# Kernel optimization log

Hardware: AMD Instinct MI355X
Metric: run time of the kernel (lower is better)

The kernel has to match this reference:

```python
import jax, jax.numpy as jnp
import numpy as np

W_CHAMFER = (1.0, 1.0, 1.0)
W_LAPLACE = 0.5
W_MOVE = 0.1
W_EDGE = 0.1
W_NORMAL = 1.6e-4
W_CONST = 1.0
LAP_CONST = (0.2, 1.0, 1.0)
EPS = 1e-12


def _normalize(x):
    # F.normalize(x, dim=-1): x / max(||x||, eps)
    n = jnp.sqrt(jnp.sum(x * x, axis=-1, keepdims=True))
    return x / jnp.maximum(n, EPS)


def _pairwise_sq(x, y):
    # x: (B,N,3), y: (B,M,3) -> (B,N,M) squared distances, GEMM form
    x2 = jnp.sum(x * x, -1)
    y2 = jnp.sum(y * y, -1)
    xy = jnp.einsum('bnd,bmd->bnm', x, y)
    return x2[:, :, None] + y2[:, None, :] - 2.0 * xy


def _laplace_coord(pts, lap_idx):
    # pts: (B,V,3); lap_idx: (V,10) = [8 neighbor idx (-1 invalid), self, count]
    idx = lap_idx[:, :8]
    mask = idx < 0
    safe = jnp.where(mask, 0, idx)
    nbrs = pts[:, safe]                                  # (B,V,8,3)
    nbrs = jnp.where(mask[None, :, :, None], 0.0, nbrs)
    count = lap_idx[:, -1].astype(pts.dtype)
    return pts - nbrs.sum(2) / count[None, :, None]


def setup_inputs():
    key = jax.random.key(0)
    B, M = 2, 8192
    Vs = (642, 2562, 10242)
    Es = (1920, 7680, 30720)
    ks = jax.random.split(key, 3 + 4 * 3)
    inp = {}
    inp['gt_coord'] = jax.random.normal(ks[0], (B, M, 3), jnp.float32)
    inp['gt_normal'] = _normalize(jax.random.normal(ks[1], (B, M, 3), jnp.float32))
    for i, (V, E) in enumerate(zip(Vs, Es)):
        k0, k1, k2, k3 = ks[3 + 4 * i], ks[4 + 4 * i], ks[5 + 4 * i], ks[6 + 4 * i]
        inp[f'pred_coord_{i}'] = jax.random.normal(k0, (B, V, 3), jnp.float32)
        inp[f'pred_before_{i}'] = inp[f'pred_coord_{i}'] + 0.05 * jax.random.normal(k1, (B, V, 3), jnp.float32)
        inp[f'edges_{i}'] = jax.random.randint(k2, (E, 2), 0, V)
        nbr = jax.random.randint(k3, (V, 8), 0, V)
        nbr = nbr.at[:, 6:].set(-1)                      # 6 valid neighbors, 2 invalid slots
        self_idx = jnp.arange(V)[:, None]
        count = jnp.full((V, 1), 6)
        inp[f'laplace_idx_{i}'] = jnp.concatenate([nbr, self_idx, count], axis=1)
    return inp


def reference(pred_coord_0, pred_coord_1, pred_coord_2, pred_before_0, pred_before_1, pred_before_2, gt_coord, gt_normal, laplace_idx_0, laplace_idx_1, laplace_idx_2, edges_0, edges_1, edges_2):
    preds = (pred_coord_0, pred_coord_1, pred_coord_2)
    befores = (pred_before_0, pred_before_1, pred_before_2)
    laps = (laplace_idx_0, laplace_idx_1, laplace_idx_2)
    edges_all = (edges_0, edges_1, edges_2)
    chamfer_loss = 0.0
    edge_loss = 0.0
    normal_loss = 0.0
    lap_loss = 0.0
    move_loss = 0.0
    for i in range(3):
        pred, before, lap_idx, edges = preds[i], befores[i], laps[i], edges_all[i]
        # shared pairwise distance matrix for chamfer + knn (original recomputes)
        d = _pairwise_sq(pred, gt_coord)                 # (B,V,M)
        chamfer_loss = chamfer_loss + W_CHAMFER[i] * (jnp.mean(jnp.min(d, axis=1)) + jnp.mean(jnp.min(d, axis=2)))
        knn_idx = jnp.argmin(d, axis=2)                  # (B,V): nearest gt per pred pt
        e0, e1 = edges[:, 0], edges[:, 1]
        evec = _normalize(pred[:, e0] - pred[:, e1])     # (B,E,3)
        # faithful to torch: knn.idx.flatten() then index_select -> only batch-0
        # indices ever selected since edge ids < V
        sel = knn_idx.reshape(-1)[e0]
        nrm = _normalize(gt_normal[:, sel])              # (B,E,3)
        normal_loss = normal_loss + jnp.mean(jnp.abs(jnp.sum(evec * nrm, axis=2)))
        edge_loss = edge_loss + 3.0 * jnp.mean((pred[:, e0] - pred[:, e1]) ** 2)
        l1 = _laplace_coord(before, lap_idx)
        l2 = _laplace_coord(pred, lap_idx)
        lap_loss = lap_loss + LAP_CONST[i] * 3.0 * jnp.mean((l1 - l2) ** 2)
        if i > 0:
            move_loss = move_loss + LAP_CONST[i] * 3.0 * jnp.mean((before - pred) ** 2)
    loss = chamfer_loss + W_LAPLACE * lap_loss + W_MOVE * move_loss + W_EDGE * edge_loss + W_NORMAL * normal_loss
    return W_CONST * loss
```

## Files before the change

kernel.cpp:

```cpp
#include <hip/hip_runtime.h>


#define DEV __device__ __forceinline__

typedef __attribute__((ext_vector_type(8))) short bs8;
typedef __attribute__((ext_vector_type(4))) float f32x4;

#define WS_GT   65536
#define WS_VP   1114112
#define WS_PA   2916352
#define WS_PB   6520832
#define WS_PAu  2916352
#define WS_PBu  3028992

DEV unsigned long long umin64(unsigned long long a, unsigned long long b) { return a < b ? a : b; }

DEV float blockReduceSum256(float v) {
    #pragma unroll
    for (int o = 32; o > 0; o >>= 1) v += __shfl_down(v, o, 64);
    __shared__ float red4[4];
    int wid = threadIdx.x >> 6;
    if ((threadIdx.x & 63) == 0) red4[wid] = v;
    __syncthreads();
    return (threadIdx.x == 0) ? (red4[0] + red4[1] + red4[2] + red4[3]) : 0.0f;
}

DEV void split3(float u, unsigned short& h, unsigned short& m, unsigned short& l) {
    unsigned a = __float_as_uint(u);
    h = (unsigned short)(a >> 16);
    float r1 = u - __uint_as_float(a & 0xFFFF0000u);
    unsigned bb = __float_as_uint(r1);
    m = (unsigned short)(bb >> 16);
    float r2 = r1 - __uint_as_float(bb & 0xFFFF0000u);
    l = (unsigned short)(__float_as_uint(r2) >> 16);
}

DEV void packGT(const float* __restrict__ gp, char* dst) {
    float x = gp[0], y = gp[1], z = gp[2];
    unsigned short hx,mx,lx, hy,my,ly, hz,mz,lz, nh,nm,nl;
    split3(x,hx,mx,lx); split3(y,hy,my,ly); split3(z,hz,mz,lz);
    float n = fmaf(x,x,fmaf(y,y,z*z));
    split3(n,nh,nm,nl);
    const short ONE = (short)0x3F80;
    bs8 w0 = {(short)hx,(short)hx,(short)mx,(short)hx,(short)lx,(short)mx,(short)hy,(short)hy};
    bs8 w1 = {(short)my,(short)hy,(short)ly,(short)my,(short)hz,(short)hz,(short)mz,(short)hz};
    bs8 w2 = {(short)lz,(short)mz,(short)nh,(short)nm,(short)nl,ONE,ONE,ONE};
    bs8 w3 = {0,0,0,0,0,0,0,0};
    *(bs8*)(dst)       = w0;
    *(bs8*)(dst + 256) = w1;
    *(bs8*)(dst + 512) = w2;
    *(bs8*)(dst + 768) = w3;
}

DEV void packVERT(const float* __restrict__ pp, char* dst) {
    float x = pp[0], y = pp[1], z = pp[2];
    unsigned short hx,mx,lx, hy,my,ly, hz,mz,lz, nh,nm,nl;
    split3(-2.f*x,hx,mx,lx); split3(-2.f*y,hy,my,ly); split3(-2.f*z,hz,mz,lz);
    float n = fmaf(x,x,fmaf(y,y,z*z));
    split3(n,nh,nm,nl);
    const short ONE = (short)0x3F80;
    bs8 w0 = {(short)hx,(short)mx,(short)hx,(short)lx,(short)hx,(short)mx,(short)hy,(short)my};
    bs8 w1 = {(short)hy,(short)ly,(short)hy,(short)my,(short)hz,(short)mz,(short)hz,(short)lz};
    bs8 w2 = {(short)hz,(short)mz,ONE,ONE,ONE,(short)nh,(short)nm,(short)nl};
    bs8 w3 = {0,0,0,0,0,0,0,0};
    *(bs8*)(dst)       = w0;
    *(bs8*)(dst + 256) = w1;
    *(bs8*)(dst + 512) = w2;
    *(bs8*)(dst + 768) = w3;
}

__global__ __launch_bounds__(256) void kPack(
    const float* __restrict__ p0, const float* __restrict__ p1, const float* __restrict__ p2,
    const float* __restrict__ gt, char* ws)
{
    int idx = blockIdx.x * 256 + threadIdx.x;
    if (idx < 16384) {
        packGT(gt + (size_t)idx * 3, ws + WS_GT + (size_t)(idx >> 4) * 1024 + (idx & 15) * 16);
    } else if (idx < 44544) {
        int s = idx - 16384;
        int b = s >= 14080 ? 1 : 0;
        int q = s - b * 14080;
        int V, padOff; const float* predL;
        if (q < 768)       { V = 642;   padOff = 0;    predL = p0; }
        else if (q < 3584) { V = 2562;  padOff = 768;  predL = p1; }
        else               { V = 10242; padOff = 3584; predL = p2; }
        int u = q - padOff;
        int v = u - (u >= V ? V : 0);
        packVERT(predL + ((size_t)b * V + v) * 3,
                 ws + WS_VP + (size_t)(s >> 4) * 1024 + (s & 15) * 16);
    }
}

template<bool B0>
DEV void mfmaLoop(const char* SA, const char* SB, char* VML,
                  float (&gmin)[4][4], int embedBase, unsigned embedMask)
{
    const int tid = threadIdx.x;
    const int w = tid >> 6, L = tid & 63, lr = L & 15, lg = L >> 4;
    const char* abase = SA + (w * 4) * 1024 + lg * 256 + lr * 16;
    bs8 af[4];
    #pragma unroll
    for (int g = 0; g < 4; g++) af[g] = *(const bs8*)(abase + g * 1024);
    const f32x4 zero = {0.f, 0.f, 0.f, 0.f};
    const char* bbase = SB + lg * 256 + lr * 16;
    bs8 bf = *(const bs8*)(bbase);
    #pragma unroll 2
    for (int vg = 0; vg < 16; vg++) {
        bs8 bfn = bf;
        if (vg < 15) bfn = *(const bs8*)(bbase + (vg + 1) * 1024);
        float vmin = 3.0e38f;
        int code = embedBase;
        #pragma unroll
        for (int gg = 0; gg < 4; gg++) {
            f32x4 acc = __builtin_amdgcn_mfma_f32_16x16x32_bf16(af[gg], bf, zero, 0, 0, 0);
            gmin[gg][0] = fminf(gmin[gg][0], acc[0]);
            gmin[gg][1] = fminf(gmin[gg][1], acc[1]);
            gmin[gg][2] = fminf(gmin[gg][2], acc[2]);
            gmin[gg][3] = fminf(gmin[gg][3], acc[3]);
            float t = fminf(fminf(acc[0], acc[1]), fminf(acc[2], acc[3]));
            if (B0) {
                t = fmaxf(t, 0.0f);
                t = __uint_as_float((__float_as_uint(t) & embedMask) | (unsigned)code);
                code += 4;
            }
            vmin = fminf(vmin, t);
        }
        vmin = fminf(vmin, __shfl_xor(vmin, 16));
        vmin = fminf(vmin, __shfl_xor(vmin, 32));
        if (lg == 0) *(float*)(VML + ((vg * 16 + lr) * 4 + w) * 4) = vmin;
        bf = bfn;
    }
}

template<bool STORE>
__global__ __launch_bounds__(256, 4) void kMega2(
    const float* __restrict__ p0, const float* __restrict__ p1, const float* __restrict__ p2,
    const float* __restrict__ b0p, const float* __restrict__ b1p, const float* __restrict__ b2p,
    const int* __restrict__ l0, const int* __restrict__ l1, const int* __restrict__ l2,
    char* ws)
{
    extern __shared__ char smem[];
    int bid = blockIdx.x;
    if (bid == 0 && threadIdx.x == 0) { *(float*)ws = 0.f; *(unsigned*)(ws + 4) = 0u; }
    if (bid < 128) {
        float c = 0.0f;
        int idx = bid * 256 + threadIdx.x;
        if (idx < 26892) {
            int level, V, t;
            const float *pred, *bef; const int* lap;
            if (idx < 1284)      { level = 0; V = 642;   pred = p0; bef = b0p; lap = l0; t = idx; }
            else if (idx < 6408) { level = 1; V = 2562;  pred = p1; bef = b1p; lap = l1; t = idx - 1284; }
            else                 { level = 2; V = 10242; pred = p2; bef = b2p; lap = l2; t = idx - 6408; }
            int b = t / V;
            int v = t - b * V;
            const float* P  = pred + ((size_t)b * V + v) * 3;
            const float* Bf = bef  + ((size_t)b * V + v) * 3;
            float dx = Bf[0] - P[0], dy = Bf[1] - P[1], dz = Bf[2] - P[2];
            float sx = 0.f, sy = 0.f, sz = 0.f;
            const int* Lp = lap + v * 10;
            #pragma unroll
            for (int j = 0; j < 8; j++) {
                int n = Lp[j];
                if (n >= 0) {
                    const float* Pn = pred + ((size_t)b * V + n) * 3;
                    const float* Bn = bef  + ((size_t)b * V + n) * 3;
                    sx += Bn[0] - Pn[0]; sy += Bn[1] - Pn[1]; sz += Bn[2] - Pn[2];
                }
            }
            float invc = 1.0f / (float)Lp[9];
            float lx = dx - sx * invc, ly = dy - sy * invc, lz = dz - sz * invc;
            float sl = fmaf(lx, lx, fmaf(ly, ly, lz * lz));
            float sm = fmaf(dx, dx, fmaf(dy, dy, dz * dz));
            float lapc = (level == 0) ? 0.2f : 1.0f;
            float iBV = 1.0f / (2.0f * (float)V);
            c = sl * (0.5f * lapc * iBV) + ((level > 0) ? sm * (0.1f * lapc * iBV) : 0.0f);
        }
        c = blockReduceSum256(c);
        if (threadIdx.x == 0) ((float*)(ws + 8))[bid] = c;
        return;
    }
    int cid = bid - 128;
    int gtt = cid & 31;
    int t2 = cid >> 5;
    int b = t2 >= 55 ? 1 : 0;
    int vt = t2 - 55 * b;
    int lvl, vtl, V, padOff, tb;
    if (vt < 3)       { lvl = 0; vtl = vt;      V = 642;   padOff = 0;    tb = 0; }
    else if (vt < 14) { lvl = 1; vtl = vt - 3;  V = 2562;  padOff = 768;  tb = 3; }
    else              { lvl = 2; vtl = vt - 14; V = 10242; padOff = 3584; tb = 14; }
    char* SA  = smem;
    char* SB  = smem + 16384;
    char* VML = smem + 32768;
    int tid = threadIdx.x;
    {
        const char* gsrc = ws + WS_GT + ((size_t)b * 8192 + gtt * 256) * 64;
        const char* vsrc = ws + WS_VP + ((size_t)(b * 14080 + padOff + vtl * 256)) * 64;
        #pragma unroll
        for (int j = 0; j < 4; j++) {
            *(bs8*)(SA + j * 4096 + tid * 16) = *(const bs8*)(gsrc + j * 4096 + (size_t)tid * 16);
            *(bs8*)(SB + j * 4096 + tid * 16) = *(const bs8*)(vsrc + j * 4096 + (size_t)tid * 16);
        }
    }
    __syncthreads();
    float gmin[4][4];
    #pragma unroll
    for (int g = 0; g < 4; g++) {
        gmin[g][0] = 3.0e38f; gmin[g][1] = 3.0e38f; gmin[g][2] = 3.0e38f; gmin[g][3] = 3.0e38f;
    }
    int w = tid >> 6, L = tid & 63, lg = L >> 4;
    if (b == 0) {
        unsigned mask = STORE ? 0xFFFFFFC0u : 0xFFFFF800u;
        int eb = w * 16 + lg + (STORE ? 0 : (gtt << 6));
        mfmaLoop<true>(SA, SB, VML, gmin, eb, mask);
    } else {
        mfmaLoop<false>(SA, SB, VML, gmin, 0, 0u);
    }
    __syncthreads();
    float* GML = (float*)smem;
    #pragma unroll
    for (int gg = 0; gg < 4; gg++) {
        #pragma unroll
        for (int r = 0; r < 4; r++)
            GML[(w * 64 + gg * 16 + lg * 4 + r) * 17 + (L & 15)] = gmin[gg][r];
    }
    __syncthreads();
    {
        float4 vv = *(float4*)(VML + tid * 16);
        float pv = fminf(fminf(vv.x, vv.y), fminf(vv.z, vv.w));
        int vs = b * 14080 + padOff + vtl * 256 + tid;
        if (STORE) {
            ((float*)(ws + WS_PA))[(size_t)gtt * 28160 + vs] = pv;
        } else {
            if (vtl * 256 + tid < V)
                atomicMin((unsigned*)(ws + WS_PAu) + vs, __float_as_uint(fmaxf(pv, 0.0f)));
        }
    }
    {
        float q = 3.0e38f;
        #pragma unroll
        for (int cc = 0; cc < 16; cc++)
            q = fminf(q, GML[tid * 17 + ((cc + tid) & 15)]);
        if (STORE) {
            ((float*)(ws + WS_PB))[(size_t)(b * 55 + tb + vtl) * 8192 + gtt * 256 + tid] = q;
        } else {
            atomicMin((unsigned*)(ws + WS_PBu) + (((b * 3 + lvl) << 13) + gtt * 256 + tid),
                      __float_as_uint(fmaxf(q, 0.0f)));
        }
    }
}

template<bool STORE>
__global__ __launch_bounds__(256) void kCombine2(
    const float* __restrict__ p0, const float* __restrict__ p1, const float* __restrict__ p2,
    const float* __restrict__ gt, char* ws)
{
    int bid = blockIdx.x, tid = threadIdx.x;
    float c = 0.0f;
    if (bid == 302) {
        if (tid < 128) c = ((float*)(ws + 8))[tid];
    } else {
        int idx = bid * 256 + tid;
        if (idx < 28160) {
            int b = idx >= 14080 ? 1 : 0;
            int q = idx - b * 14080;
            int lvl, V, lvlOff, padOff; const float* predL; float inv;
            if (q < 768)       { lvl=0; V=642;   padOff=0;    lvlOff=0;    predL=p0; inv=1.f/1284.f; }
            else if (q < 3584) { lvl=1; V=2562;  padOff=768;  lvlOff=642;  predL=p1; inv=1.f/5124.f; }
            else               { lvl=2; V=10242; padOff=3584; lvlOff=3204; predL=p2; inv=1.f/20484.f; }
            int v = q - padOff;
            if (v < V) {
                float best; int bt = 0; unsigned bits;
                if (STORE) {
                    const float* P = (const float*)(ws + WS_PA) + idx;
                    best = P[0];
                    #pragma unroll 8
                    for (int t = 1; t < 32; t++) {
                        float u = P[(size_t)t * 28160];
                        if (u < best) { best = u; bt = t; }
                    }
                    bits = __float_as_uint(best);
                } else {
                    bits = ((const unsigned*)(ws + WS_PAu))[idx];
                    best = __uint_as_float(bits);
                    bt = (bits >> 6) & 31;
                }
                float d;
                if (b == 0) {
                    int code = bits & 0x3F;
                    int m0 = bt * 256 + code * 4;
                    const float* pp = predL + (size_t)v * 3;
                    float px = pp[0], py = pp[1], pz = pp[2];
                    float bd = 3.0e38f; int bm = m0;
                    #pragma unroll
                    for (int u2 = 0; u2 < 4; u2++) {
                        const float* gp = gt + (size_t)(m0 + u2) * 3;
                        float dx = px - gp[0], dy = py - gp[1], dz = pz - gp[2];
                        float dd = fmaf(dx, dx, fmaf(dy, dy, dz * dz));
                        if (dd < bd) { bd = dd; bm = m0 + u2; }
                    }
                    ((int*)(ws + 1024))[lvlOff + v] = bm;
                    d = bd;
                } else {
                    d = best;
                }
                c = d * inv;
            }
        } else if (idx < 77312) {
            int r = idx - 28160;
            int b = r >= 24576 ? 1 : 0;
            int rem = r - b * 24576;
            int lvl = rem >> 13, m = rem & 8191;
            float d;
            if (STORE) {
                int nt = lvl == 0 ? 3 : (lvl == 1 ? 11 : 41);
                int tb = lvl == 0 ? 0 : (lvl == 1 ? 3 : 14);
                const float* P = (const float*)(ws + WS_PB) + (size_t)(b * 55 + tb) * 8192 + m;
                d = P[0];
                for (int k2 = 1; k2 < nt; k2++) d = fminf(d, P[(size_t)k2 * 8192]);
            } else {
                d = __uint_as_float(((const unsigned*)(ws + WS_PBu))[((b * 3 + lvl) << 13) + m]);
            }
            c = d * (1.f / 16384.f);
        }
    }
    c = blockReduceSum256(c);
    if (tid == 0) atomicAdd((float*)ws, c);
}

__global__ __launch_bounds__(256) void kEdgeOut(
    const float* __restrict__ p0, const float* __restrict__ p1, const float* __restrict__ p2,
    const int* __restrict__ e0p, const int* __restrict__ e1p, const int* __restrict__ e2p,
    const float* __restrict__ gtn, char* ws, float* __restrict__ out)
{
    const int* knn = (const int*)(ws + 1024);
    int idx = blockIdx.x * 256 + threadIdx.x;
    float c = 0.0f;
    {
        int E, V, lvlOff, t;
        const float* pred; const int* edges;
        if (idx < 3840)       { E = 1920;  V = 642;   lvlOff = 0;    pred = p0; edges = e0p; t = idx; }
        else if (idx < 19200) { E = 7680;  V = 2562;  lvlOff = 642;  pred = p1; edges = e1p; t = idx - 3840; }
        else                  { E = 30720; V = 10242; lvlOff = 3204; pred = p2; edges = e2p; t = idx - 19200; }
        int b = t / E;
        int e = t % E;
        int a0 = edges[e * 2 + 0];
        int a1 = edges[e * 2 + 1];
        const float* P = pred + (size_t)b * V * 3;
        float dx = P[a0 * 3 + 0] - P[a1 * 3 + 0];
        float dy = P[a0 * 3 + 1] - P[a1 * 3 + 1];
        float dz = P[a0 * 3 + 2] - P[a1 * 3 + 2];
        float sq = fmaf(dx, dx, fmaf(dy, dy, dz * dz));
        float inv = 1.0f / fmaxf(sqrtf(sq), 1e-12f);
        int sel = knn[lvlOff + a0];
        const float* nr = gtn + ((size_t)b * 8192 + sel) * 3;
        float nx = nr[0], ny = nr[1], nz = nr[2];
        float invn = 1.0f / fmaxf(sqrtf(fmaf(nx, nx, fmaf(ny, ny, nz * nz))), 1e-12f);
        float dotv = fmaf(dx, nx, fmaf(dy, ny, dz * nz)) * inv * invn;
        float iBE = 1.0f / (2.0f * (float)E);
        c = sq * (0.1f * iBE) + fabsf(dotv) * (0.00016f * iBE);
    }
    c = blockReduceSum256(c);
    if (threadIdx.x == 0) {
        atomicAdd((float*)ws, c);
        __threadfence();
        unsigned t = atomicAdd((unsigned*)(ws + 4), 1u);
        if (t == 314u) out[0] = atomicAdd((float*)ws, 0.0f);
    }
}

extern "C" void kernel_launch(void* const* d_in, const int* in_sizes, int n_in,
                              void* d_out, int out_size, void* d_ws, size_t ws_size,
                              hipStream_t stream) {
    const float *gt, *gtn, *pred[3], *bef[3];
    const int *edg[3], *lapx[3];
    if (in_sizes[0] == 49152) {
        gt  = (const float*)d_in[0];
        gtn = (const float*)d_in[1];
        for (int i = 0; i < 3; i++) {
            pred[i] = (const float*)d_in[2 + 4 * i];
            bef[i]  = (const float*)d_in[3 + 4 * i];
            edg[i]  = (const int*)  d_in[4 + 4 * i];
            lapx[i] = (const int*)  d_in[5 + 4 * i];
        }
    } else {
        for (int i = 0; i < 3; i++) pred[i] = (const float*)d_in[i];
        for (int i = 0; i < 3; i++) bef[i]  = (const float*)d_in[3 + i];
        gt  = (const float*)d_in[6];
        gtn = (const float*)d_in[7];
        for (int i = 0; i < 3; i++) lapx[i] = (const int*)d_in[8 + i];
        for (int i = 0; i < 3; i++) edg[i]  = (const int*)d_in[11 + i];
    }

    char* ws = (char*)d_ws;
    bool store = ws_size >= (size_t)10125312;

    kPack<<<174, 256, 0, stream>>>(pred[0], pred[1], pred[2], gt, ws);
    if (store) {
        kMega2<true><<<3648, 256, 36864, stream>>>(pred[0], pred[1], pred[2],
                                                   bef[0], bef[1], bef[2],
                                                   lapx[0], lapx[1], lapx[2], ws);
        kCombine2<true><<<303, 256, 0, stream>>>(pred[0], pred[1], pred[2], gt, ws);
    } else {
        hipMemsetAsync(ws + WS_PAu, 0xFF, 3225600 - WS_PAu, stream);
        kMega2<false><<<3648, 256, 36864, stream>>>(pred[0], pred[1], pred[2],
                                                    bef[0], bef[1], bef[2],
                                                    lapx[0], lapx[1], lapx[2], ws);
        kCombine2<false><<<303, 256, 0, stream>>>(pred[0], pred[1], pred[2], gt, ws);
    }
    kEdgeOut<<<315, 256, 0, stream>>>(pred[0], pred[1], pred[2],
                                      edg[0], edg[1], edg[2], gtn, ws, (float*)d_out);
}
```

Before: 134.5 us.

## Load MFMA operands directly from global and reduce gt minima with shuffles

The chamfer MFMA kernel now reads its packed GT and vertex fragments straight from global memory instead of staging them through 32 KB of LDS. The per-GT minimum is reduced across lanes with xor shuffles and written out by one lane, replacing the padded LDS transpose and its barrier. Dynamic LDS drops to 4 KB and the occupancy hint rises from 4 to 6 blocks. In exchange, the B fragments in the inner loop are now repeated global/L2 loads instead of LDS reads, which may expose memory latency.

```diff
diff --git a/kernel.cpp b/kernel.cpp
--- a/kernel.cpp
+++ b/kernel.cpp
@@ -12,8 +12,6 @@
 #define WS_PB   6520832
 #define WS_PAu  2916352
 #define WS_PBu  3028992
-
-DEV unsigned long long umin64(unsigned long long a, unsigned long long b) { return a < b ? a : b; }
 
 DEV float blockReduceSum256(float v) {
     #pragma unroll
@@ -92,22 +90,20 @@
 }
 
 template<bool B0>
-DEV void mfmaLoop(const char* SA, const char* SB, char* VML,
+DEV void mfmaLoop(const char* abase, const char* vbase, char* VML,
                   float (&gmin)[4][4], int embedBase, unsigned embedMask)
 {
     const int tid = threadIdx.x;
-    const int w = tid >> 6, L = tid & 63, lr = L & 15, lg = L >> 4;
-    const char* abase = SA + (w * 4) * 1024 + lg * 256 + lr * 16;
+    const int w = tid >> 6, L = tid & 63, lr = L & 15;
     bs8 af[4];
     #pragma unroll
     for (int g = 0; g < 4; g++) af[g] = *(const bs8*)(abase + g * 1024);
     const f32x4 zero = {0.f, 0.f, 0.f, 0.f};
-    const char* bbase = SB + lg * 256 + lr * 16;
-    bs8 bf = *(const bs8*)(bbase);
+    bs8 bf = *(const bs8*)(vbase);
     #pragma unroll 2
     for (int vg = 0; vg < 16; vg++) {
         bs8 bfn = bf;
-        if (vg < 15) bfn = *(const bs8*)(bbase + (vg + 1) * 1024);
+        if (vg < 15) bfn = *(const bs8*)(vbase + (vg + 1) * 1024);
         float vmin = 3.0e38f;
         int code = embedBase;
         #pragma unroll
@@ -127,13 +123,13 @@
         }
         vmin = fminf(vmin, __shfl_xor(vmin, 16));
         vmin = fminf(vmin, __shfl_xor(vmin, 32));
-        if (lg == 0) *(float*)(VML + ((vg * 16 + lr) * 4 + w) * 4) = vmin;
+        if (L < 16) *(float*)(VML + ((vg * 16 + lr) * 4 + w) * 4) = vmin;
         bf = bfn;
     }
 }
 
 template<bool STORE>
-__global__ __launch_bounds__(256, 4) void kMega2(
+__global__ __launch_bounds__(256, 6) void kMega2(
     const float* __restrict__ p0, const float* __restrict__ p1, const float* __restrict__ p2,
     const float* __restrict__ b0p, const float* __restrict__ b1p, const float* __restrict__ b2p,
     const int* __restrict__ l0, const int* __restrict__ l1, const int* __restrict__ l2,
@@ -188,63 +184,65 @@
     if (vt < 3)       { lvl = 0; vtl = vt;      V = 642;   padOff = 0;    tb = 0; }
     else if (vt < 14) { lvl = 1; vtl = vt - 3;  V = 2562;  padOff = 768;  tb = 3; }
     else              { lvl = 2; vtl = vt - 14; V = 10242; padOff = 3584; tb = 14; }
-    char* SA  = smem;
-    char* SB  = smem + 16384;
-    char* VML = smem + 32768;
     int tid = threadIdx.x;
-    {
-        const char* gsrc = ws + WS_GT + ((size_t)b * 8192 + gtt * 256) * 64;
-        const char* vsrc = ws + WS_VP + ((size_t)(b * 14080 + padOff + vtl * 256)) * 64;
-        #pragma unroll
-        for (int j = 0; j < 4; j++) {
-            *(bs8*)(SA + j * 4096 + tid * 16) = *(const bs8*)(gsrc + j * 4096 + (size_t)tid * 16);
-            *(bs8*)(SB + j * 4096 + tid * 16) = *(const bs8*)(vsrc + j * 4096 + (size_t)tid * 16);
-        }
-    }
-    __syncthreads();
+    int w = tid >> 6, L = tid & 63, lr = L & 15, lg = L >> 4;
+    const char* abase = ws + WS_GT + (size_t)(b * 512 + gtt * 16 + w * 4) * 1024
+                        + lg * 256 + lr * 16;
+    int slotBase = b * 14080 + padOff + vtl * 256;
+    const char* vbase = ws + WS_VP + (size_t)(slotBase >> 4) * 1024 + lg * 256 + lr * 16;
+    char* VML = smem;
     float gmin[4][4];
     #pragma unroll
     for (int g = 0; g < 4; g++) {
         gmin[g][0] = 3.0e38f; gmin[g][1] = 3.0e38f; gmin[g][2] = 3.0e38f; gmin[g][3] = 3.0e38f;
     }
-    int w = tid >> 6, L = tid & 63, lg = L >> 4;
     if (b == 0) {
         unsigned mask = STORE ? 0xFFFFFFC0u : 0xFFFFF800u;
         int eb = w * 16 + lg + (STORE ? 0 : (gtt << 6));
-        mfmaLoop<true>(SA, SB, VML, gmin, eb, mask);
+        mfmaLoop<true>(abase, vbase, VML, gmin, eb, mask);
     } else {
-        mfmaLoop<false>(SA, SB, VML, gmin, 0, 0u);
-    }
-    __syncthreads();
-    float* GML = (float*)smem;
-    #pragma unroll
-    for (int gg = 0; gg < 4; gg++) {
+        mfmaLoop<false>(abase, vbase, VML, gmin, 0, 0u);
+    }
+    {
         #pragma unroll
-        for (int r = 0; r < 4; r++)
-            GML[(w * 64 + gg * 16 + lg * 4 + r) * 17 + (L & 15)] = gmin[gg][r];
+        for (int gg = 0; gg < 4; gg++) {
+            #pragma unroll
+            for (int r = 0; r < 4; r++) {
+                float v = gmin[gg][r];
+                v = fminf(v, __shfl_xor(v, 1));
+                v = fminf(v, __shfl_xor(v, 2));
+                v = fminf(v, __shfl_xor(v, 4));
+                v = fminf(v, __shfl_xor(v, 8));
+                gmin[gg][r] = v;
+            }
+        }
+        if (lr == 0) {
+            #pragma unroll
+            for (int gg = 0; gg < 4; gg++) {
+                int row = w * 64 + gg * 16 + lg * 4;
+                if (STORE) {
+                    float4 q = make_float4(gmin[gg][0], gmin[gg][1], gmin[gg][2], gmin[gg][3]);
+                    *(float4*)((float*)(ws + WS_PB)
+                        + (size_t)(b * 55 + tb + vtl) * 8192 + gtt * 256 + row) = q;
+                } else {
+                    unsigned* dst = (unsigned*)(ws + WS_PBu) + (((b * 3 + lvl) << 13) + gtt * 256 + row);
+                    #pragma unroll
+                    for (int r = 0; r < 4; r++)
+                        atomicMin(dst + r, __float_as_uint(fmaxf(gmin[gg][r], 0.0f)));
+                }
+            }
+        }
     }
     __syncthreads();
     {
         float4 vv = *(float4*)(VML + tid * 16);
         float pv = fminf(fminf(vv.x, vv.y), fminf(vv.z, vv.w));
-        int vs = b * 14080 + padOff + vtl * 256 + tid;
+        int vs = slotBase + tid;
         if (STORE) {
             ((float*)(ws + WS_PA))[(size_t)gtt * 28160 + vs] = pv;
         } else {
             if (vtl * 256 + tid < V)
                 atomicMin((unsigned*)(ws + WS_PAu) + vs, __float_as_uint(fmaxf(pv, 0.0f)));
-        }
-    }
-    {
-        float q = 3.0e38f;
-        #pragma unroll
-        for (int cc = 0; cc < 16; cc++)
-            q = fminf(q, GML[tid * 17 + ((cc + tid) & 15)]);
-        if (STORE) {
-            ((float*)(ws + WS_PB))[(size_t)(b * 55 + tb + vtl) * 8192 + gtt * 256 + tid] = q;
-        } else {
-            atomicMin((unsigned*)(ws + WS_PBu) + (((b * 3 + lvl) << 13) + gtt * 256 + tid),
-                      __float_as_uint(fmaxf(q, 0.0f)));
         }
     }
 }
@@ -396,15 +394,15 @@
 
     kPack<<<174, 256, 0, stream>>>(pred[0], pred[1], pred[2], gt, ws);
     if (store) {
-        kMega2<true><<<3648, 256, 36864, stream>>>(pred[0], pred[1], pred[2],
-                                                   bef[0], bef[1], bef[2],
-                                                   lapx[0], lapx[1], lapx[2], ws);
+        kMega2<true><<<3648, 256, 4096, stream>>>(pred[0], pred[1], pred[2],
+                                                  bef[0], bef[1], bef[2],
+                                                  lapx[0], lapx[1], lapx[2], ws);
         kCombine2<true><<<303, 256, 0, stream>>>(pred[0], pred[1], pred[2], gt, ws);
     } else {
         hipMemsetAsync(ws + WS_PAu, 0xFF, 3225600 - WS_PAu, stream);
-        kMega2<false><<<3648, 256, 36864, stream>>>(pred[0], pred[1], pred[2],
-                                                    bef[0], bef[1], bef[2],
-                                                    lapx[0], lapx[1], lapx[2], ws);
+        kMega2<false><<<3648, 256, 4096, stream>>>(pred[0], pred[1], pred[2],
+                                                   bef[0], bef[1], bef[2],
+                                                   lapx[0], lapx[1], lapx[2], ws);
         kCombine2<false><<<303, 256, 0, stream>>>(pred[0], pred[1], pred[2], gt, ws);
     }
     kEdgeOut<<<315, 256, 0, stream>>>(pred[0], pred[1], pred[2],
```

New measurement: 139.7 us. +3.9%, slower.
